# Performance work log

Measured on AMD Instinct MI355X. Metric: run time of the kernel, lower is better.

The kernel has to match this reference:

```python
import jax, jax.numpy as jnp
import numpy as np

EPS = 1e-7  # K.epsilon()

def squash(s):
    # s: [B, J, D]
    sq_norm = jnp.sum(jnp.square(s), axis=-1, keepdims=True)
    scale = sq_norm / (1.0 + sq_norm) / jnp.sqrt(sq_norm + EPS)
    return scale * s

def setup_inputs() -> dict:
    key = jax.random.key(0)
    k1, k2 = jax.random.split(key)
    B, I, Din = 128, 2048, 8
    J, D = 16, 16
    inputs = jax.random.normal(k1, (B, I, Din), dtype=jnp.float32)
    # glorot-uniform-ish scale for W
    limit = np.sqrt(6.0 / (Din + D)).astype(np.float32)
    W = jax.random.uniform(k2, (J, I, D, Din), dtype=jnp.float32, minval=-limit, maxval=limit)
    return {"inputs": inputs, "W": W}

def reference(inputs, W):
    # inputs: [B, I, Din]; W: [J, I, D, Din]
    num_routings = 3
    # inputs_hat[b,j,i,d] = sum_f W[j,i,d,f] * inputs[b,i,f]
    u_hat = jnp.einsum('bif,jidf->bjid', inputs, W)  # [B, J, I, D]
    B, J, I, D = u_hat.shape
    b = jnp.zeros((B, J, I), dtype=u_hat.dtype)
    v = None
    for r in range(num_routings):
        c = jax.nn.softmax(b, axis=1)                 # softmax over output capsules (dim=1)
        s = jnp.einsum('bji,bjid->bjd', c, u_hat)     # weighted sum over input capsules
        v = squash(s)                                 # [B, J, D]
        if r < num_routings - 1:
            b = b + jnp.einsum('bjd,bjid->bji', v, u_hat)  # agreement update
    return v
```

## Files before the change

### kernel.cpp

```cpp
#include <hip/hip_runtime.h>
#include <math.h>

#define B_   128
#define I_   2048
#define F_   8
#define J_   16
#define D_   16
#define JD   256
#define BT   16
#define NBT  (B_/BT)
#define SROW 257

typedef _Float16 f16;
typedef _Float16 f16x8 __attribute__((ext_vector_type(8)));
typedef _Float16 f16x4 __attribute__((ext_vector_type(4)));
typedef float    f32x4 __attribute__((ext_vector_type(4)));

#if defined(__has_builtin)
#  if __has_builtin(__builtin_amdgcn_permlane32_swap)
#    define HAVE_PLS32 1
#  endif
#endif

template <int CTRL>
__device__ __forceinline__ float dpp_add(float v) {
    int t = __builtin_amdgcn_update_dpp(0, __float_as_int(v), CTRL, 0xF, 0xF, true);
    return v + __int_as_float(t);
}
__device__ __forceinline__ float row_sum16(float v) {
    v = dpp_add<0x128>(v);
    v = dpp_add<0x124>(v);
    v = dpp_add<0x122>(v);
    v = dpp_add<0x121>(v);
    return v;
}

__device__ __forceinline__ float fold16(float p) {
    return p + __int_as_float(__builtin_amdgcn_ds_swizzle(__float_as_int(p), 0x401F));
}
__device__ __forceinline__ float fold32(float p) {
#ifdef HAVE_PLS32
    auto r = __builtin_amdgcn_permlane32_swap(__float_as_int(p), __float_as_int(p),
                                              false, false);
    return __int_as_float(r[0]) + __int_as_float(r[1]);
#else
    return p + __shfl_xor(p, 32);
#endif
}

__global__ __launch_bounds__(256) void cvt_f16(const float* __restrict__ W,
                                               const float* __restrict__ x,
                                               f16* __restrict__ Wt,
                                               f16* __restrict__ xt) {
    const size_t NW = (size_t)J_ * I_ * D_ * F_;
    const size_t NX = (size_t)B_ * I_ * F_;
    size_t k = ((size_t)blockIdx.x * 256 + threadIdx.x) * 4;
    if (k < NW) {
        float4 a = *reinterpret_cast<const float4*>(W + k);
        f16x4 h = {(f16)a.x, (f16)a.y, (f16)a.z, (f16)a.w};
        *reinterpret_cast<f16x4*>(Wt + k) = h;
    } else {
        size_t k2 = k - NW;
        if (k2 < NX) {
            float4 a = *reinterpret_cast<const float4*>(x + k2);
            f16x4 h = {(f16)a.x, (f16)a.y, (f16)a.z, (f16)a.w};
            *reinterpret_cast<f16x4*>(xt + k2) = h;
        }
    }
}

template <int IT, int PASS>
__global__ __launch_bounds__(256) void caps_pass(
    const f16* __restrict__ Wt,
    const f16* __restrict__ xt,
    const float* __restrict__ vsum,
    f16* __restrict__ sp)
{
    const int it = blockIdx.x, bg = blockIdx.y;
    const int i0 = it * IT, b0 = bg * BT;
    const int t = threadIdx.x;
    const int w = t >> 6, l = t & 63;
    const int lb = l & 15, lq = l >> 4;

    __shared__ f16 xlds[IT][BT][F_];
    __shared__ union {
        float cl[J_ * IT * BT];
        float slds[BT * SROW];
    } sh;

    if constexpr (IT == 16) {
        const int b = t >> 4, i = t & 15;
        f16x8 v = *reinterpret_cast<const f16x8*>(
            xt + ((size_t)(b0 + b) * I_ + i0 + i) * F_);
        *reinterpret_cast<f16x8*>(&xlds[i][b][0]) = v;
    } else {
        if (t < 128) {
            const int b = t >> 3, i = t & 7;
            f16x8 v = *reinterpret_cast<const f16x8*>(
                xt + ((size_t)(b0 + b) * I_ + i0 + i) * F_);
            *reinterpret_cast<f16x8*>(&xlds[i][b][0]) = v;
        }
    }

    const f16* wp[4];
    #pragma unroll
    for (int jj = 0; jj < 4; ++jj)
        wp[jj] = Wt + (((size_t)(w * 4 + jj) * I_ + i0) * D_ + lb) * F_;

    f32x4 zero = {0.f, 0.f, 0.f, 0.f};
    f32x4 sacc[4] = {zero, zero, zero, zero};

    if constexpr (PASS == 1) {
        float4 vr[4];
        #pragma unroll
        for (int jj = 0; jj < 4; ++jj)
            vr[jj] = *reinterpret_cast<const float4*>(
                vsum + (size_t)(b0 + lb) * JD + (w * 4 + jj) * D_ + lq * 4);
        __syncthreads();

        #pragma unroll 4
        for (int il = 0; il < IT; ++il) {
            f16x8 bf = {0, 0, 0, 0, 0, 0, 0, 0};
            if (l < 16) bf = *reinterpret_cast<const f16x8*>(&xlds[il][lb][0]);
            #pragma unroll
            for (int jj = 0; jj < 4; ++jj) {
                f16x8 af = *reinterpret_cast<const f16x8*>(wp[jj] + il * (D_ * F_));
                f32x4 u = __builtin_amdgcn_mfma_f32_16x16x32_f16(af, bf, zero, 0, 0, 0);
                float p = u[0] * vr[jj].x + u[1] * vr[jj].y +
                          u[2] * vr[jj].z + u[3] * vr[jj].w;
                p = fold32(fold16(p));
                if (l < 16) sh.cl[(((w * 4 + jj) * IT) + il) * BT + lb] = p;
            }
        }
        __syncthreads();

        if (t < IT * BT) {
            const int i = t >> 4, b = t & 15;
            float e[J_];
            float mx = -1e30f;
            #pragma unroll
            for (int j = 0; j < J_; ++j) {
                e[j] = sh.cl[(j * IT + i) * BT + b];
                mx = fmaxf(mx, e[j]);
            }
            float ssum = 0.f;
            #pragma unroll
            for (int j = 0; j < J_; ++j) { e[j] = __expf(e[j] - mx); ssum += e[j]; }
            const float inv = 1.f / ssum;
            #pragma unroll
            for (int j = 0; j < J_; ++j) sh.cl[(j * IT + i) * BT + b] = e[j] * inv;
        }
        __syncthreads();
    } else {
        __syncthreads();
    }

    #pragma unroll
    for (int m = 0; m < IT / 4; ++m) {
        const int i = m * 4 + lq;
        f16x8 xf = *reinterpret_cast<const f16x8*>(&xlds[i][lb][0]);
        #pragma unroll
        for (int jj = 0; jj < 4; ++jj) {
            f16x8 bf;
            if constexpr (PASS == 1) {
                const float cf = sh.cl[(((w * 4 + jj) * IT) + i) * BT + lb];
                const f16 ch = (f16)cf;
                bf = xf * ch;
            } else {
                bf = xf;
            }
            f16x8 af = *reinterpret_cast<const f16x8*>(wp[jj] + i * (D_ * F_));
            sacc[jj] = __builtin_amdgcn_mfma_f32_16x16x32_f16(af, bf, sacc[jj], 0, 0, 0);
        }
    }

    __syncthreads();

    #pragma unroll
    for (int jj = 0; jj < 4; ++jj) {
        if constexpr (PASS == 0) sacc[jj] *= 0.0625f;
        const int j = w * 4 + jj;
        #pragma unroll
        for (int r = 0; r < 4; ++r)
            sh.slds[lb * SROW + j * D_ + lq * 4 + r] = sacc[jj][r];
    }
    __syncthreads();
    {
        const int b = t >> 4, seg = t & 15;
        float o[16];
        #pragma unroll
        for (int k = 0; k < 16; ++k)
            o[k] = sh.slds[b * SROW + seg * 16 + k];
        f16x8 o0 = {(f16)o[0], (f16)o[1], (f16)o[2],  (f16)o[3],
                    (f16)o[4], (f16)o[5], (f16)o[6],  (f16)o[7]};
        f16x8 o1 = {(f16)o[8], (f16)o[9], (f16)o[10], (f16)o[11],
                    (f16)o[12], (f16)o[13], (f16)o[14], (f16)o[15]};
        f16* dst = sp + ((size_t)it * B_ + b0 + b) * JD + seg * 16;
        *reinterpret_cast<f16x8*>(dst) = o0;
        *reinterpret_cast<f16x8*>(dst + 8) = o1;
    }
}

template <int NITT, int MODE>
__global__ __launch_bounds__(512) void caps_reduce(
    const f16* __restrict__ sp,
    const float* __restrict__ vA,
    float* __restrict__ vout)
{
    const int b = blockIdx.x, jh = blockIdx.y;
    const int t = threadIdx.x;
    const int g = t >> 4, c8 = t & 15;
    constexpr int ITS = NITT / 32;

    float acc[8] = {0.f, 0.f, 0.f, 0.f, 0.f, 0.f, 0.f, 0.f};
    const f16* base = sp + ((size_t)(g * ITS) * B_ + b) * JD + jh * 128 + c8 * 8;
    #pragma unroll
    for (int k = 0; k < ITS; ++k) {
        f16x8 v = *reinterpret_cast<const f16x8*>(base + (size_t)k * B_ * JD);
        #pragma unroll
        for (int e = 0; e < 8; ++e) acc[e] += (float)v[e];
    }

    __shared__ float lds[32][128];
    #pragma unroll
    for (int e = 0; e < 8; ++e) lds[g][c8 * 8 + e] = acc[e];
    __syncthreads();

    if (t < 128) {
        float a = 0.f;
        #pragma unroll
        for (int gg = 0; gg < 32; ++gg) a += lds[gg][t];
        const float sq = row_sum16(a * a);
        const float scale = sq / (1.f + sq) * rsqrtf(sq + 1e-7f);
        float v = scale * a;
        const int jd = jh * 128 + t;
        if (MODE == 1) v += vA[(size_t)b * JD + jd];
        vout[(size_t)b * JD + jd] = v;
    }
}

extern "C" void kernel_launch(void* const* d_in, const int* in_sizes, int n_in,
                              void* d_out, int out_size, void* d_ws,
                              size_t ws_size, hipStream_t stream) {
    const float* x = (const float*)d_in[0];
    const float* W = (const float*)d_in[1];
    float* out = (float*)d_out;

    const size_t NW = (size_t)J_ * I_ * D_ * F_;
    const size_t NX = (size_t)B_ * I_ * F_;

    f16* Wt = (f16*)d_ws;
    f16* xt = Wt + NW;
    f16* sp = xt + NX;

    const int TOT4 = (int)((NW + NX) / 4);

    const size_t need8 = NW * 2 + NX * 2 +
                         (size_t)256 * B_ * JD * 2 + 2 * (size_t)B_ * JD * 4;
    dim3 rgrid(B_, 2), rblk(512);

    if (ws_size >= need8) {
        float* vA = (float*)(sp + (size_t)256 * B_ * JD);
        float* vB = vA + (size_t)B_ * JD;
        dim3 grid(I_ / 8, NBT), blk(256);
        cvt_f16<<<TOT4 / 256, 256, 0, stream>>>(W, x, Wt, xt);
        caps_pass<8, 0><<<grid, blk, 0, stream>>>(Wt, xt, nullptr, sp);
        caps_reduce<256, 0><<<rgrid, rblk, 0, stream>>>(sp, nullptr, vA);
        caps_pass<8, 1><<<grid, blk, 0, stream>>>(Wt, xt, vA, sp);
        caps_reduce<256, 1><<<rgrid, rblk, 0, stream>>>(sp, vA, vB);
        caps_pass<8, 1><<<grid, blk, 0, stream>>>(Wt, xt, vB, sp);
        caps_reduce<256, 2><<<rgrid, rblk, 0, stream>>>(sp, nullptr, out);
    } else {
        float* vA = (float*)(sp + (size_t)128 * B_ * JD);
        float* vB = vA + (size_t)B_ * JD;
        dim3 grid(I_ / 16, NBT), blk(256);
        cvt_f16<<<TOT4 / 256, 256, 0, stream>>>(W, x, Wt, xt);
        caps_pass<16, 0><<<grid, blk, 0, stream>>>(Wt, xt, nullptr, sp);
        caps_reduce<128, 0><<<rgrid, rblk, 0, stream>>>(sp, nullptr, vA);
        caps_pass<16, 1><<<grid, blk, 0, stream>>>(Wt, xt, vA, sp);
        caps_reduce<128, 1><<<rgrid, rblk, 0, stream>>>(sp, vA, vB);
        caps_pass<16, 1><<<grid, blk, 0, stream>>>(Wt, xt, vB, sp);
        caps_reduce<128, 2><<<rgrid, rblk, 0, stream>>>(sp, nullptr, out);
    }
}
```

Baseline: 81.59 us.

## Fuse fp16 conversion into first pass, widen batch tile, reuse W fragments in registers

Removes the standalone fp32-to-fp16 conversion kernel: pass 0 now reads fp32 W and x directly, converts them, and writes the fp16 copies for the later passes. The batch tile grows from 16 to 32 with a fixed input tile of 16, so each W fragment feeds two MFMAs and W traffic per pass is halved. W fragments loaded during the routing-logit loop are kept in registers and reused for the weighted sum. The cost is more register pressure and a larger shared-memory footprint, and the smaller-workspace fallback is dropped.

```diff
diff --git a/kernel.cpp b/kernel.cpp
--- a/kernel.cpp
+++ b/kernel.cpp
@@ -7,13 +7,16 @@
 #define J_   16
 #define D_   16
 #define JD   256
-#define BT   16
-#define NBT  (B_/BT)
+#define IT   16
+#define NIT  (I_/IT)
+#define BT   32
+#define NBG  (B_/BT)
 #define SROW 257
+#define CLS  33
+#define JSTR ((size_t)I_*D_*F_)
 
 typedef _Float16 f16;
 typedef _Float16 f16x8 __attribute__((ext_vector_type(8)));
-typedef _Float16 f16x4 __attribute__((ext_vector_type(4)));
 typedef float    f32x4 __attribute__((ext_vector_type(4)));
 
 #if defined(__has_builtin)
@@ -48,31 +51,18 @@
 #endif
 }
 
-__global__ __launch_bounds__(256) void cvt_f16(const float* __restrict__ W,
-                                               const float* __restrict__ x,
-                                               f16* __restrict__ Wt,
-                                               f16* __restrict__ xt) {
-    const size_t NW = (size_t)J_ * I_ * D_ * F_;
-    const size_t NX = (size_t)B_ * I_ * F_;
-    size_t k = ((size_t)blockIdx.x * 256 + threadIdx.x) * 4;
-    if (k < NW) {
-        float4 a = *reinterpret_cast<const float4*>(W + k);
-        f16x4 h = {(f16)a.x, (f16)a.y, (f16)a.z, (f16)a.w};
-        *reinterpret_cast<f16x4*>(Wt + k) = h;
-    } else {
-        size_t k2 = k - NW;
-        if (k2 < NX) {
-            float4 a = *reinterpret_cast<const float4*>(x + k2);
-            f16x4 h = {(f16)a.x, (f16)a.y, (f16)a.z, (f16)a.w};
-            *reinterpret_cast<f16x4*>(xt + k2) = h;
-        }
-    }
-}
-
-template <int IT, int PASS>
+__device__ __forceinline__ f16x8 cvt8(float4 a0, float4 a1) {
+    f16x8 h = {(f16)a0.x, (f16)a0.y, (f16)a0.z, (f16)a0.w,
+               (f16)a1.x, (f16)a1.y, (f16)a1.z, (f16)a1.w};
+    return h;
+}
+
+template <int PASS>
 __global__ __launch_bounds__(256) void caps_pass(
-    const f16* __restrict__ Wt,
-    const f16* __restrict__ xt,
+    const float* __restrict__ Wf,
+    const float* __restrict__ xf,
+    f16* __restrict__ Wt,
+    f16* __restrict__ xt,
     const float* __restrict__ vsum,
     f16* __restrict__ sp)
 {
@@ -84,63 +74,98 @@
 
     __shared__ f16 xlds[IT][BT][F_];
     __shared__ union {
-        float cl[J_ * IT * BT];
+        float cl[J_ * IT * CLS];
         float slds[BT * SROW];
     } sh;
 
-    if constexpr (IT == 16) {
-        const int b = t >> 4, i = t & 15;
-        f16x8 v = *reinterpret_cast<const f16x8*>(
-            xt + ((size_t)(b0 + b) * I_ + i0 + i) * F_);
-        *reinterpret_cast<f16x8*>(&xlds[i][b][0]) = v;
-    } else {
-        if (t < 128) {
-            const int b = t >> 3, i = t & 7;
-            f16x8 v = *reinterpret_cast<const f16x8*>(
-                xt + ((size_t)(b0 + b) * I_ + i0 + i) * F_);
-            *reinterpret_cast<f16x8*>(&xlds[i][b][0]) = v;
-        }
-    }
-
-    const f16* wp[4];
-    #pragma unroll
-    for (int jj = 0; jj < 4; ++jj)
-        wp[jj] = Wt + (((size_t)(w * 4 + jj) * I_ + i0) * D_ + lb) * F_;
-
-    f32x4 zero = {0.f, 0.f, 0.f, 0.f};
-    f32x4 sacc[4] = {zero, zero, zero, zero};
+    {
+        const int b = t >> 3, ii = (t & 7) * 2;
+        #pragma unroll
+        for (int k = 0; k < 2; ++k) {
+            const size_t off = ((size_t)(b0 + b) * I_ + i0 + ii + k) * F_;
+            f16x8 h;
+            if constexpr (PASS == 0) {
+                const float4* src = reinterpret_cast<const float4*>(xf + off);
+                h = cvt8(src[0], src[1]);
+                *reinterpret_cast<f16x8*>(xt + off) = h;
+            } else {
+                h = *reinterpret_cast<const f16x8*>(xt + off);
+            }
+            *reinterpret_cast<f16x8*>(&xlds[ii + k][b][0]) = h;
+        }
+    }
+
+    f16x8 afc[4][4];
+
+    if constexpr (PASS == 0) {
+        #pragma unroll
+        for (int m = 0; m < 4; ++m)
+            #pragma unroll
+            for (int jj = 0; jj < 4; ++jj) {
+                const size_t off =
+                    (((size_t)(w * 4 + jj) * I_ + i0 + m * 4 + lq) * D_ + lb) * F_;
+                const float4* src = reinterpret_cast<const float4*>(Wf + off);
+                f16x8 h = cvt8(src[0], src[1]);
+                afc[m][jj] = h;
+                if (bg == 0) *reinterpret_cast<f16x8*>(Wt + off) = h;
+            }
+    }
+    __syncthreads();
+
+    const f32x4 zero = {0.f, 0.f, 0.f, 0.f};
 
     if constexpr (PASS == 1) {
-        float4 vr[4];
+        float4 vrh[2][4];
+        #pragma unroll
+        for (int bh = 0; bh < 2; ++bh)
+            #pragma unroll
+            for (int jj = 0; jj < 4; ++jj)
+                vrh[bh][jj] = *reinterpret_cast<const float4*>(
+                    vsum + (size_t)(b0 + bh * 16 + lb) * JD +
+                    (w * 4 + jj) * D_ + lq * 4);
+
+        const f16* wp[4];
         #pragma unroll
         for (int jj = 0; jj < 4; ++jj)
-            vr[jj] = *reinterpret_cast<const float4*>(
-                vsum + (size_t)(b0 + lb) * JD + (w * 4 + jj) * D_ + lq * 4);
-        __syncthreads();
-
-        #pragma unroll 4
+            wp[jj] = Wt + (((size_t)(w * 4 + jj) * I_ + i0) * D_ + lb) * F_;
+
+        #pragma unroll
         for (int il = 0; il < IT; ++il) {
-            f16x8 bf = {0, 0, 0, 0, 0, 0, 0, 0};
-            if (l < 16) bf = *reinterpret_cast<const f16x8*>(&xlds[il][lb][0]);
+            f16x8 bf0 = {0, 0, 0, 0, 0, 0, 0, 0};
+            f16x8 bf1 = {0, 0, 0, 0, 0, 0, 0, 0};
+            if (l < 16) {
+                bf0 = *reinterpret_cast<const f16x8*>(&xlds[il][lb][0]);
+                bf1 = *reinterpret_cast<const f16x8*>(&xlds[il][16 + lb][0]);
+            }
             #pragma unroll
             for (int jj = 0; jj < 4; ++jj) {
                 f16x8 af = *reinterpret_cast<const f16x8*>(wp[jj] + il * (D_ * F_));
-                f32x4 u = __builtin_amdgcn_mfma_f32_16x16x32_f16(af, bf, zero, 0, 0, 0);
-                float p = u[0] * vr[jj].x + u[1] * vr[jj].y +
-                          u[2] * vr[jj].z + u[3] * vr[jj].w;
-                p = fold32(fold16(p));
-                if (l < 16) sh.cl[(((w * 4 + jj) * IT) + il) * BT + lb] = p;
+                if ((il & 3) == lq) afc[il >> 2][jj] = af;
+                f32x4 u0 = __builtin_amdgcn_mfma_f32_16x16x32_f16(af, bf0, zero, 0, 0, 0);
+                float p0 = u0[0] * vrh[0][jj].x + u0[1] * vrh[0][jj].y +
+                           u0[2] * vrh[0][jj].z + u0[3] * vrh[0][jj].w;
+                p0 = fold32(fold16(p0));
+                f32x4 u1 = __builtin_amdgcn_mfma_f32_16x16x32_f16(af, bf1, zero, 0, 0, 0);
+                float p1 = u1[0] * vrh[1][jj].x + u1[1] * vrh[1][jj].y +
+                           u1[2] * vrh[1][jj].z + u1[3] * vrh[1][jj].w;
+                p1 = fold32(fold16(p1));
+                if (l < 16) {
+                    sh.cl[((w * 4 + jj) * IT + il) * CLS + lb] = p0;
+                    sh.cl[((w * 4 + jj) * IT + il) * CLS + 16 + lb] = p1;
+                }
             }
         }
         __syncthreads();
 
-        if (t < IT * BT) {
-            const int i = t >> 4, b = t & 15;
+        #pragma unroll
+        for (int hh = 0; hh < 2; ++hh) {
+            const int item = hh * 256 + t;
+            const int i = item >> 5, b = item & 31;
             float e[J_];
             float mx = -1e30f;
             #pragma unroll
             for (int j = 0; j < J_; ++j) {
-                e[j] = sh.cl[(j * IT + i) * BT + b];
+                e[j] = sh.cl[(j * IT + i) * CLS + b];
                 mx = fmaxf(mx, e[j]);
             }
             float ssum = 0.f;
@@ -148,56 +173,67 @@
             for (int j = 0; j < J_; ++j) { e[j] = __expf(e[j] - mx); ssum += e[j]; }
             const float inv = 1.f / ssum;
             #pragma unroll
-            for (int j = 0; j < J_; ++j) sh.cl[(j * IT + i) * BT + b] = e[j] * inv;
+            for (int j = 0; j < J_; ++j) sh.cl[(j * IT + i) * CLS + b] = e[j] * inv;
         }
         __syncthreads();
-    } else {
-        __syncthreads();
-    }
-
-    #pragma unroll
-    for (int m = 0; m < IT / 4; ++m) {
+    }
+
+    f32x4 sacc[4][2];
+    #pragma unroll
+    for (int jj = 0; jj < 4; ++jj) { sacc[jj][0] = zero; sacc[jj][1] = zero; }
+
+    #pragma unroll
+    for (int m = 0; m < 4; ++m) {
         const int i = m * 4 + lq;
-        f16x8 xf = *reinterpret_cast<const f16x8*>(&xlds[i][lb][0]);
+        f16x8 xf0 = *reinterpret_cast<const f16x8*>(&xlds[i][lb][0]);
+        f16x8 xf1 = *reinterpret_cast<const f16x8*>(&xlds[i][16 + lb][0]);
         #pragma unroll
         for (int jj = 0; jj < 4; ++jj) {
-            f16x8 bf;
+            f16x8 b0v, b1v;
             if constexpr (PASS == 1) {
-                const float cf = sh.cl[(((w * 4 + jj) * IT) + i) * BT + lb];
-                const f16 ch = (f16)cf;
-                bf = xf * ch;
+                const f16 c0 = (f16)sh.cl[((w * 4 + jj) * IT + i) * CLS + lb];
+                const f16 c1 = (f16)sh.cl[((w * 4 + jj) * IT + i) * CLS + 16 + lb];
+                b0v = xf0 * c0;
+                b1v = xf1 * c1;
             } else {
-                bf = xf;
-            }
-            f16x8 af = *reinterpret_cast<const f16x8*>(wp[jj] + i * (D_ * F_));
-            sacc[jj] = __builtin_amdgcn_mfma_f32_16x16x32_f16(af, bf, sacc[jj], 0, 0, 0);
-        }
-    }
-
+                b0v = xf0;
+                b1v = xf1;
+            }
+            sacc[jj][0] = __builtin_amdgcn_mfma_f32_16x16x32_f16(
+                afc[m][jj], b0v, sacc[jj][0], 0, 0, 0);
+            sacc[jj][1] = __builtin_amdgcn_mfma_f32_16x16x32_f16(
+                afc[m][jj], b1v, sacc[jj][1], 0, 0, 0);
+        }
+    }
     __syncthreads();
 
     #pragma unroll
     for (int jj = 0; jj < 4; ++jj) {
-        if constexpr (PASS == 0) sacc[jj] *= 0.0625f;
-        const int j = w * 4 + jj;
-        #pragma unroll
-        for (int r = 0; r < 4; ++r)
-            sh.slds[lb * SROW + j * D_ + lq * 4 + r] = sacc[jj][r];
+        #pragma unroll
+        for (int bh = 0; bh < 2; ++bh) {
+            f32x4 sv = sacc[jj][bh];
+            if constexpr (PASS == 0) sv *= 0.0625f;
+            const int j = w * 4 + jj;
+            #pragma unroll
+            for (int r = 0; r < 4; ++r)
+                sh.slds[(bh * 16 + lb) * SROW + j * D_ + lq * 4 + r] = sv[r];
+        }
     }
     __syncthreads();
     {
-        const int b = t >> 4, seg = t & 15;
-        float o[16];
-        #pragma unroll
-        for (int k = 0; k < 16; ++k)
-            o[k] = sh.slds[b * SROW + seg * 16 + k];
-        f16x8 o0 = {(f16)o[0], (f16)o[1], (f16)o[2],  (f16)o[3],
-                    (f16)o[4], (f16)o[5], (f16)o[6],  (f16)o[7]};
-        f16x8 o1 = {(f16)o[8], (f16)o[9], (f16)o[10], (f16)o[11],
-                    (f16)o[12], (f16)o[13], (f16)o[14], (f16)o[15]};
-        f16* dst = sp + ((size_t)it * B_ + b0 + b) * JD + seg * 16;
-        *reinterpret_cast<f16x8*>(dst) = o0;
-        *reinterpret_cast<f16x8*>(dst + 8) = o1;
+        const int b = t >> 3, seg = t & 7;
+        float o[32];
+        #pragma unroll
+        for (int k = 0; k < 32; ++k)
+            o[k] = sh.slds[b * SROW + seg * 32 + k];
+        f16* dst = sp + ((size_t)it * B_ + b0 + b) * JD + seg * 32;
+        #pragma unroll
+        for (int q = 0; q < 4; ++q) {
+            f16x8 h = {(f16)o[q * 8 + 0], (f16)o[q * 8 + 1], (f16)o[q * 8 + 2],
+                       (f16)o[q * 8 + 3], (f16)o[q * 8 + 4], (f16)o[q * 8 + 5],
+                       (f16)o[q * 8 + 6], (f16)o[q * 8 + 7]};
+            *reinterpret_cast<f16x8*>(dst + q * 8) = h;
+        }
     }
 }
 
@@ -248,38 +284,21 @@
 
     const size_t NW = (size_t)J_ * I_ * D_ * F_;
     const size_t NX = (size_t)B_ * I_ * F_;
+    const size_t NSP = (size_t)NIT * B_ * JD;
 
     f16* Wt = (f16*)d_ws;
     f16* xt = Wt + NW;
     f16* sp = xt + NX;
-
-    const int TOT4 = (int)((NW + NX) / 4);
-
-    const size_t need8 = NW * 2 + NX * 2 +
-                         (size_t)256 * B_ * JD * 2 + 2 * (size_t)B_ * JD * 4;
+    float* vA = (float*)(sp + NSP);
+    float* vB = vA + (size_t)B_ * JD;
+
+    dim3 grid(NIT, NBG), blk(256);
     dim3 rgrid(B_, 2), rblk(512);
 
-    if (ws_size >= need8) {
-        float* vA = (float*)(sp + (size_t)256 * B_ * JD);
-        float* vB = vA + (size_t)B_ * JD;
-        dim3 grid(I_ / 8, NBT), blk(256);
-        cvt_f16<<<TOT4 / 256, 256, 0, stream>>>(W, x, Wt, xt);
-        caps_pass<8, 0><<<grid, blk, 0, stream>>>(Wt, xt, nullptr, sp);
-        caps_reduce<256, 0><<<rgrid, rblk, 0, stream>>>(sp, nullptr, vA);
-        caps_pass<8, 1><<<grid, blk, 0, stream>>>(Wt, xt, vA, sp);
-        caps_reduce<256, 1><<<rgrid, rblk, 0, stream>>>(sp, vA, vB);
-        caps_pass<8, 1><<<grid, blk, 0, stream>>>(Wt, xt, vB, sp);
-        caps_reduce<256, 2><<<rgrid, rblk, 0, stream>>>(sp, nullptr, out);
-    } else {
-        float* vA = (float*)(sp + (size_t)128 * B_ * JD);
-        float* vB = vA + (size_t)B_ * JD;
-        dim3 grid(I_ / 16, NBT), blk(256);
-        cvt_f16<<<TOT4 / 256, 256, 0, stream>>>(W, x, Wt, xt);
-        caps_pass<16, 0><<<grid, blk, 0, stream>>>(Wt, xt, nullptr, sp);
-        caps_reduce<128, 0><<<rgrid, rblk, 0, stream>>>(sp, nullptr, vA);
-        caps_pass<16, 1><<<grid, blk, 0, stream>>>(Wt, xt, vA, sp);
-        caps_reduce<128, 1><<<rgrid, rblk, 0, stream>>>(sp, vA, vB);
-        caps_pass<16, 1><<<grid, blk, 0, stream>>>(Wt, xt, vB, sp);
-        caps_reduce<128, 2><<<rgrid, rblk, 0, stream>>>(sp, nullptr, out);
-    }
-}
+    caps_pass<0><<<grid, blk, 0, stream>>>(W, x, Wt, xt, nullptr, sp);
+    caps_reduce<NIT, 0><<<rgrid, rblk, 0, stream>>>(sp, nullptr, vA);
+    caps_pass<1><<<grid, blk, 0, stream>>>(nullptr, nullptr, Wt, xt, vA, sp);
+    caps_reduce<NIT, 1><<<rgrid, rblk, 0, stream>>>(sp, vA, vB);
+    caps_pass<1><<<grid, blk, 0, stream>>>(nullptr, nullptr, Wt, xt, vB, sp);
+    caps_reduce<NIT, 2><<<rgrid, rblk, 0, stream>>>(sp, nullptr, out);
+}
```

Result: slower. 123.6 us (+51.5%).

## Fuse fp32-to-fp16 conversion into the first routing pass and fix IT=16

Applied to the files above, without the earlier changes.

Removes the standalone conversion kernel and has the first routing pass read fp32 W and x directly. It converts them in registers, runs the uniform-coefficient MFMA sum, and writes the fp16 copies for later passes. Only the first batch group stores W. The tile is fixed at IT=16, dropping the IT=8 path the launcher took when the workspace was large enough. This saves one launch and one full read of W. In exchange, pass0 reads fp32 W eight times, once per batch group, and halves the partial-sum buffer and reduction depth.

```diff
diff --git a/kernel.cpp b/kernel.cpp
--- a/kernel.cpp
+++ b/kernel.cpp
@@ -7,13 +7,14 @@
 #define J_   16
 #define D_   16
 #define JD   256
+#define IT   16
+#define NIT  (I_/IT)
 #define BT   16
-#define NBT  (B_/BT)
+#define NBG  (B_/BT)
 #define SROW 257
 
 typedef _Float16 f16;
 typedef _Float16 f16x8 __attribute__((ext_vector_type(8)));
-typedef _Float16 f16x4 __attribute__((ext_vector_type(4)));
 typedef float    f32x4 __attribute__((ext_vector_type(4)));
 
 #if defined(__has_builtin)
@@ -48,29 +49,83 @@
 #endif
 }
 
-__global__ __launch_bounds__(256) void cvt_f16(const float* __restrict__ W,
-                                               const float* __restrict__ x,
-                                               f16* __restrict__ Wt,
-                                               f16* __restrict__ xt) {
-    const size_t NW = (size_t)J_ * I_ * D_ * F_;
-    const size_t NX = (size_t)B_ * I_ * F_;
-    size_t k = ((size_t)blockIdx.x * 256 + threadIdx.x) * 4;
-    if (k < NW) {
-        float4 a = *reinterpret_cast<const float4*>(W + k);
-        f16x4 h = {(f16)a.x, (f16)a.y, (f16)a.z, (f16)a.w};
-        *reinterpret_cast<f16x4*>(Wt + k) = h;
-    } else {
-        size_t k2 = k - NW;
-        if (k2 < NX) {
-            float4 a = *reinterpret_cast<const float4*>(x + k2);
-            f16x4 h = {(f16)a.x, (f16)a.y, (f16)a.z, (f16)a.w};
-            *reinterpret_cast<f16x4*>(xt + k2) = h;
+__device__ __forceinline__ f16x8 cvt8(float4 a0, float4 a1) {
+    f16x8 h = {(f16)a0.x, (f16)a0.y, (f16)a0.z, (f16)a0.w,
+               (f16)a1.x, (f16)a1.y, (f16)a1.z, (f16)a1.w};
+    return h;
+}
+
+__global__ __launch_bounds__(256) void caps_pass0(
+    const float* __restrict__ Wf,
+    const float* __restrict__ xf,
+    f16* __restrict__ Wt,
+    f16* __restrict__ xt,
+    f16* __restrict__ sp)
+{
+    const int it = blockIdx.x, bg = blockIdx.y;
+    const int i0 = it * IT, b0 = bg * BT;
+    const int t = threadIdx.x;
+    const int w = t >> 6, l = t & 63;
+    const int lb = l & 15, lq = l >> 4;
+
+    __shared__ f16   xlds[IT][BT][F_];
+    __shared__ float slds[BT * SROW];
+
+    {
+        const int b = t >> 4, i = t & 15;
+        const size_t off = ((size_t)(b0 + b) * I_ + i0 + i) * F_;
+        const float4* src = reinterpret_cast<const float4*>(xf + off);
+        f16x8 h = cvt8(src[0], src[1]);
+        *reinterpret_cast<f16x8*>(xt + off) = h;
+        *reinterpret_cast<f16x8*>(&xlds[i][b][0]) = h;
+    }
+    __syncthreads();
+
+    const f32x4 zero = {0.f, 0.f, 0.f, 0.f};
+    f32x4 sacc[4] = {zero, zero, zero, zero};
+
+    #pragma unroll
+    for (int m = 0; m < 4; ++m) {
+        const int i = m * 4 + lq;
+        f16x8 xv = *reinterpret_cast<const f16x8*>(&xlds[i][lb][0]);
+        #pragma unroll
+        for (int jj = 0; jj < 4; ++jj) {
+            const size_t off =
+                (((size_t)(w * 4 + jj) * I_ + i0 + i) * D_ + lb) * F_;
+            const float4* sw = reinterpret_cast<const float4*>(Wf + off);
+            f16x8 af = cvt8(sw[0], sw[1]);
+            if (bg == 0) *reinterpret_cast<f16x8*>(Wt + off) = af;
+            sacc[jj] = __builtin_amdgcn_mfma_f32_16x16x32_f16(
+                af, xv, sacc[jj], 0, 0, 0);
         }
     }
-}
-
-template <int IT, int PASS>
-__global__ __launch_bounds__(256) void caps_pass(
+
+    #pragma unroll
+    for (int jj = 0; jj < 4; ++jj) {
+        f32x4 sv = sacc[jj] * 0.0625f;
+        const int j = w * 4 + jj;
+        #pragma unroll
+        for (int r = 0; r < 4; ++r)
+            slds[lb * SROW + j * D_ + lq * 4 + r] = sv[r];
+    }
+    __syncthreads();
+    {
+        const int b = t >> 4, seg = t & 15;
+        float o[16];
+        #pragma unroll
+        for (int k = 0; k < 16; ++k)
+            o[k] = slds[b * SROW + seg * 16 + k];
+        f16x8 o0 = {(f16)o[0], (f16)o[1], (f16)o[2],  (f16)o[3],
+                    (f16)o[4], (f16)o[5], (f16)o[6],  (f16)o[7]};
+        f16x8 o1 = {(f16)o[8], (f16)o[9], (f16)o[10], (f16)o[11],
+                    (f16)o[12], (f16)o[13], (f16)o[14], (f16)o[15]};
+        f16* dst = sp + ((size_t)it * B_ + b0 + b) * JD + seg * 16;
+        *reinterpret_cast<f16x8*>(dst) = o0;
+        *reinterpret_cast<f16x8*>(dst + 8) = o1;
+    }
+}
+
+__global__ __launch_bounds__(256) void caps_pass1(
     const f16* __restrict__ Wt,
     const f16* __restrict__ xt,
     const float* __restrict__ vsum,
@@ -88,18 +143,11 @@
         float slds[BT * SROW];
     } sh;
 
-    if constexpr (IT == 16) {
+    {
         const int b = t >> 4, i = t & 15;
         f16x8 v = *reinterpret_cast<const f16x8*>(
             xt + ((size_t)(b0 + b) * I_ + i0 + i) * F_);
         *reinterpret_cast<f16x8*>(&xlds[i][b][0]) = v;
-    } else {
-        if (t < 128) {
-            const int b = t >> 3, i = t & 7;
-            f16x8 v = *reinterpret_cast<const f16x8*>(
-                xt + ((size_t)(b0 + b) * I_ + i0 + i) * F_);
-            *reinterpret_cast<f16x8*>(&xlds[i][b][0]) = v;
-        }
     }
 
     const f16* wp[4];
@@ -107,78 +155,67 @@
     for (int jj = 0; jj < 4; ++jj)
         wp[jj] = Wt + (((size_t)(w * 4 + jj) * I_ + i0) * D_ + lb) * F_;
 
-    f32x4 zero = {0.f, 0.f, 0.f, 0.f};
+    const f32x4 zero = {0.f, 0.f, 0.f, 0.f};
     f32x4 sacc[4] = {zero, zero, zero, zero};
 
-    if constexpr (PASS == 1) {
-        float4 vr[4];
-        #pragma unroll
-        for (int jj = 0; jj < 4; ++jj)
-            vr[jj] = *reinterpret_cast<const float4*>(
-                vsum + (size_t)(b0 + lb) * JD + (w * 4 + jj) * D_ + lq * 4);
-        __syncthreads();
-
-        #pragma unroll 4
-        for (int il = 0; il < IT; ++il) {
-            f16x8 bf = {0, 0, 0, 0, 0, 0, 0, 0};
-            if (l < 16) bf = *reinterpret_cast<const f16x8*>(&xlds[il][lb][0]);
-            #pragma unroll
-            for (int jj = 0; jj < 4; ++jj) {
-                f16x8 af = *reinterpret_cast<const f16x8*>(wp[jj] + il * (D_ * F_));
-                f32x4 u = __builtin_amdgcn_mfma_f32_16x16x32_f16(af, bf, zero, 0, 0, 0);
-                float p = u[0] * vr[jj].x + u[1] * vr[jj].y +
-                          u[2] * vr[jj].z + u[3] * vr[jj].w;
-                p = fold32(fold16(p));
-                if (l < 16) sh.cl[(((w * 4 + jj) * IT) + il) * BT + lb] = p;
-            }
+    float4 vr[4];
+    #pragma unroll
+    for (int jj = 0; jj < 4; ++jj)
+        vr[jj] = *reinterpret_cast<const float4*>(
+            vsum + (size_t)(b0 + lb) * JD + (w * 4 + jj) * D_ + lq * 4);
+    __syncthreads();
+
+    #pragma unroll 4
+    for (int il = 0; il < IT; ++il) {
+        f16x8 bf = {0, 0, 0, 0, 0, 0, 0, 0};
+        if (l < 16) bf = *reinterpret_cast<const f16x8*>(&xlds[il][lb][0]);
+        #pragma unroll
+        for (int jj = 0; jj < 4; ++jj) {
+            f16x8 af = *reinterpret_cast<const f16x8*>(wp[jj] + il * (D_ * F_));
+            f32x4 u = __builtin_amdgcn_mfma_f32_16x16x32_f16(af, bf, zero, 0, 0, 0);
+            float p = u[0] * vr[jj].x + u[1] * vr[jj].y +
+                      u[2] * vr[jj].z + u[3] * vr[jj].w;
+            p = fold32(fold16(p));
+            if (l < 16) sh.cl[(((w * 4 + jj) * IT) + il) * BT + lb] = p;
         }
-        __syncthreads();
-
-        if (t < IT * BT) {
-            const int i = t >> 4, b = t & 15;
-            float e[J_];
-            float mx = -1e30f;
-            #pragma unroll
-            for (int j = 0; j < J_; ++j) {
-                e[j] = sh.cl[(j * IT + i) * BT + b];
-                mx = fmaxf(mx, e[j]);
-            }
-            float ssum = 0.f;
-            #pragma unroll
-            for (int j = 0; j < J_; ++j) { e[j] = __expf(e[j] - mx); ssum += e[j]; }
-            const float inv = 1.f / ssum;
-            #pragma unroll
-            for (int j = 0; j < J_; ++j) sh.cl[(j * IT + i) * BT + b] = e[j] * inv;
+    }
+    __syncthreads();
+
+    {
+        const int i = t >> 4, b = t & 15;
+        float e[J_];
+        float mx = -1e30f;
+        #pragma unroll
+        for (int j = 0; j < J_; ++j) {
+            e[j] = sh.cl[(j * IT + i) * BT + b];
+            mx = fmaxf(mx, e[j]);
         }
-        __syncthreads();
-    } else {
-        __syncthreads();
-    }
-
-    #pragma unroll
-    for (int m = 0; m < IT / 4; ++m) {
+        float ssum = 0.f;
+        #pragma unroll
+        for (int j = 0; j < J_; ++j) { e[j] = __expf(e[j] - mx); ssum += e[j]; }
+        const float inv = 1.f / ssum;
+        #pragma unroll
+        for (int j = 0; j < J_; ++j) sh.cl[(j * IT + i) * BT + b] = e[j] * inv;
+    }
+    __syncthreads();
+
+    #pragma unroll
+    for (int m = 0; m < 4; ++m) {
         const int i = m * 4 + lq;
-        f16x8 xf = *reinterpret_cast<const f16x8*>(&xlds[i][lb][0]);
+        f16x8 xv = *reinterpret_cast<const f16x8*>(&xlds[i][lb][0]);
         #pragma unroll
         for (int jj = 0; jj < 4; ++jj) {
-            f16x8 bf;
-            if constexpr (PASS == 1) {
-                const float cf = sh.cl[(((w * 4 + jj) * IT) + i) * BT + lb];
-                const f16 ch = (f16)cf;
-                bf = xf * ch;
-            } else {
-                bf = xf;
-            }
+            const f16 ch = (f16)sh.cl[(((w * 4 + jj) * IT) + i) * BT + lb];
+            f16x8 bf = xv * ch;
             f16x8 af = *reinterpret_cast<const f16x8*>(wp[jj] + i * (D_ * F_));
-            sacc[jj] = __builtin_amdgcn_mfma_f32_16x16x32_f16(af, bf, sacc[jj], 0, 0, 0);
+            sacc[jj] = __builtin_amdgcn_mfma_f32_16x16x32_f16(
+                af, bf, sacc[jj], 0, 0, 0);
         }
     }
-
     __syncthreads();
 
     #pragma unroll
     for (int jj = 0; jj < 4; ++jj) {
-        if constexpr (PASS == 0) sacc[jj] *= 0.0625f;
         const int j = w * 4 + jj;
         #pragma unroll
         for (int r = 0; r < 4; ++r)
@@ -201,7 +238,7 @@
     }
 }
 
-template <int NITT, int MODE>
+template <int MODE>
 __global__ __launch_bounds__(512) void caps_reduce(
     const f16* __restrict__ sp,
     const float* __restrict__ vA,
@@ -210,7 +247,7 @@
     const int b = blockIdx.x, jh = blockIdx.y;
     const int t = threadIdx.x;
     const int g = t >> 4, c8 = t & 15;
-    constexpr int ITS = NITT / 32;
+    constexpr int ITS = NIT / 32;
 
     float acc[8] = {0.f, 0.f, 0.f, 0.f, 0.f, 0.f, 0.f, 0.f};
     const f16* base = sp + ((size_t)(g * ITS) * B_ + b) * JD + jh * 128 + c8 * 8;
@@ -248,38 +285,21 @@
 
     const size_t NW = (size_t)J_ * I_ * D_ * F_;
     const size_t NX = (size_t)B_ * I_ * F_;
+    const size_t NSP = (size_t)NIT * B_ * JD;
 
     f16* Wt = (f16*)d_ws;
     f16* xt = Wt + NW;
     f16* sp = xt + NX;
-
-    const int TOT4 = (int)((NW + NX) / 4);
-
-    const size_t need8 = NW * 2 + NX * 2 +
-                         (size_t)256 * B_ * JD * 2 + 2 * (size_t)B_ * JD * 4;
+    float* vA = (float*)(sp + NSP);
+    float* vB = vA + (size_t)B_ * JD;
+
+    dim3 grid(NIT, NBG), blk(256);
     dim3 rgrid(B_, 2), rblk(512);
 
-    if (ws_size >= need8) {
-        float* vA = (float*)(sp + (size_t)256 * B_ * JD);
-        float* vB = vA + (size_t)B_ * JD;
-        dim3 grid(I_ / 8, NBT), blk(256);
-        cvt_f16<<<TOT4 / 256, 256, 0, stream>>>(W, x, Wt, xt);
-        caps_pass<8, 0><<<grid, blk, 0, stream>>>(Wt, xt, nullptr, sp);
-        caps_reduce<256, 0><<<rgrid, rblk, 0, stream>>>(sp, nullptr, vA);
-        caps_pass<8, 1><<<grid, blk, 0, stream>>>(Wt, xt, vA, sp);
-        caps_reduce<256, 1><<<rgrid, rblk, 0, stream>>>(sp, vA, vB);
-        caps_pass<8, 1><<<grid, blk, 0, stream>>>(Wt, xt, vB, sp);
-        caps_reduce<256, 2><<<rgrid, rblk, 0, stream>>>(sp, nullptr, out);
-    } else {
-        float* vA = (float*)(sp + (size_t)128 * B_ * JD);
-        float* vB = vA + (size_t)B_ * JD;
-        dim3 grid(I_ / 16, NBT), blk(256);
-        cvt_f16<<<TOT4 / 256, 256, 0, stream>>>(W, x, Wt, xt);
-        caps_pass<16, 0><<<grid, blk, 0, stream>>>(Wt, xt, nullptr, sp);
-        caps_reduce<128, 0><<<rgrid, rblk, 0, stream>>>(sp, nullptr, vA);
-        caps_pass<16, 1><<<grid, blk, 0, stream>>>(Wt, xt, vA, sp);
-        caps_reduce<128, 1><<<rgrid, rblk, 0, stream>>>(sp, vA, vB);
-        caps_pass<16, 1><<<grid, blk, 0, stream>>>(Wt, xt, vB, sp);
-        caps_reduce<128, 2><<<rgrid, rblk, 0, stream>>>(sp, nullptr, out);
-    }
-}
+    caps_pass0<<<grid, blk, 0, stream>>>(W, x, Wt, xt, sp);
+    caps_reduce<0><<<rgrid, rblk, 0, stream>>>(sp, nullptr, vA);
+    caps_pass1<<<grid, blk, 0, stream>>>(Wt, xt, vA, sp);
+    caps_reduce<1><<<rgrid, rblk, 0, stream>>>(sp, vA, vB);
+    caps_pass1<<<grid, blk, 0, stream>>>(Wt, xt, vB, sp);
+    caps_reduce<2><<<rgrid, rblk, 0, stream>>>(sp, nullptr, out);
+}
```

Measured after the change: 82.33 us. Within noise of the previous version (+0.9%).
